# Optimization experiments

Hardware: AMD Instinct MI355X
Metric: run time of the kernel (lower is better)

Reference implementation:

```python
import jax, jax.numpy as jnp
import numpy as np

B, T, IN, H = 64, 512, 512, 512


def _lstm_scan(x_tbd, h0, c0, Wih, Whh, b):
    """Run an LSTMCell over time. x_tbd: [T,B,IN]. Returns hs [T,B,H], (h,c)."""
    def step(carry, x):
        h, c = carry
        g = x @ Wih.T + h @ Whh.T + b          # [B, 4H], gates in torch order i,f,g,o
        i, f, gg, o = jnp.split(g, 4, axis=-1)
        i = jax.nn.sigmoid(i)
        f = jax.nn.sigmoid(f)
        gg = jnp.tanh(gg)
        o = jax.nn.sigmoid(o)
        c = f * c + i * gg
        h = o * jnp.tanh(c)
        return (h, c), h
    (h, c), hs = jax.lax.scan(step, (h0, c0), x_tbd)
    return hs, h, c


def setup_inputs() -> dict:
    key = jax.random.key(0)
    ks = jax.random.split(key, 9)
    s = 1.0 / np.sqrt(H)
    inp = {
        "input": jax.random.normal(ks[0], (B, T, IN), dtype=jnp.float32),
        "enc_h": jax.random.normal(ks[1], (B, 2 * H), dtype=jnp.float32),
        "enc_c": jax.random.normal(ks[2], (B, 2 * H), dtype=jnp.float32),
        "Wih_f": jax.random.uniform(ks[3], (4 * H, IN), jnp.float32, -s, s),
        "Whh_f": jax.random.uniform(ks[4], (4 * H, H), jnp.float32, -s, s),
        "b_f": jax.random.uniform(ks[5], (4 * H,), jnp.float32, -s, s),
        "Wih_b": jax.random.uniform(ks[6], (4 * H, IN), jnp.float32, -s, s),
        "Whh_b": jax.random.uniform(ks[7], (4 * H, H), jnp.float32, -s, s),
        "b_b": jax.random.uniform(ks[8], (4 * H,), jnp.float32, -s, s),
    }
    return inp


def reference(input, enc_h, enc_c, Wih_f, Whh_f, b_f, Wih_b, Whh_b, b_b):
    # split encoder state into forward / backward halves (num_layers=1)
    h0_f, h0_b = enc_h[:, :H], enc_h[:, H:]
    c0_f, c0_b = enc_c[:, :H], enc_c[:, H:]

    x_f = jnp.swapaxes(input, 0, 1)                 # [T,B,IN]
    x_b = jnp.swapaxes(jnp.flip(input, axis=1), 0, 1)

    out_f, h_f, c_f = _lstm_scan(x_f, h0_f, c0_f, Wih_f, Whh_f, b_f)
    out_b, h_b, c_b = _lstm_scan(x_b, h0_b, c0_b, Wih_b, Whh_b, b_b)

    out_f = jnp.swapaxes(out_f, 0, 1)               # [B,T,H]
    out_b = jnp.flip(jnp.swapaxes(out_b, 0, 1), axis=1)
    out = jnp.concatenate([out_f, out_b], axis=2)   # [B,T,2H]

    h = jnp.concatenate([h_f, h_b], axis=1)         # [B,2H]
    c = jnp.concatenate([c_f, c_b], axis=1)
    return out, h, c
```

## Files before the change

### kernel.cpp

```cpp
#include <hip/hip_runtime.h>

typedef _Float16 h8 __attribute__((ext_vector_type(8)));
typedef _Float16 h4 __attribute__((ext_vector_type(4)));
typedef float    f4 __attribute__((ext_vector_type(4)));
typedef unsigned u4 __attribute__((ext_vector_type(4)));

#define NT     512
#define OUT0   33554432
#define SENT   0x7fc00000u

__device__ __forceinline__ float sigm(float x)  { return 1.0f / (1.0f + __expf(-x)); }
__device__ __forceinline__ float tanhf_(float x){ float e = __expf(2.0f * x); return 1.0f - 2.0f / (e + 1.0f); }


__global__ __launch_bounds__(256) void xconv_k(const float* __restrict__ x, _Float16* __restrict__ x16) {
    size_t i = ((size_t)blockIdx.x * 256 + threadIdx.x) * 4;
    f4 v = *(const f4*)(x + i);
    h4 o; o[0] = (_Float16)v[0]; o[1] = (_Float16)v[1]; o[2] = (_Float16)v[2]; o[3] = (_Float16)v[3];
    *(h4*)(x16 + i) = o;
}

__global__ __launch_bounds__(256) void wconv_k(const float* __restrict__ Wih_f, const float* __restrict__ Whh_f,
                                               const float* __restrict__ Wih_b, const float* __restrict__ Whh_b,
                                               _Float16* __restrict__ wcat) {
    size_t e = (size_t)blockIdx.x * 256 + threadIdx.x;
    int k4  = (int)(e & 255);
    int p   = (int)((e >> 8) & 2047);
    int dir = (int)(e >> 19);
    int gate = p & 3, j = p >> 2;
    int k = k4 * 4;
    const float* Wih = dir ? Wih_b : Wih_f;
    const float* Whh = dir ? Whh_b : Whh_f;
    f4 v;
    if (k < 512) v = *(const f4*)&Wih[((size_t)gate * 512 + j) * 512 + k];
    else         v = *(const f4*)&Whh[((size_t)gate * 512 + j) * 512 + (k - 512)];
    h4 o; o[0] = (_Float16)v[0]; o[1] = (_Float16)v[1]; o[2] = (_Float16)v[2]; o[3] = (_Float16)v[3];
    *(h4*)&wcat[(((size_t)dir * 2048) + p) * 1024 + k] = o;
}

__global__ __launch_bounds__(256) void inith_k(const float* __restrict__ enc_h, _Float16* __restrict__ h16) {
    int e = blockIdx.x * 256 + threadIdx.x;
    float v = enc_h[e];
    int b = e >> 10, q = e & 1023, dir = q >> 9, j = q & 511;
    h16[((size_t)(dir * 64 + b)) * 512 + j] = (_Float16)v;
}

__global__ __launch_bounds__(256) void fillnan_k(unsigned* __restrict__ o) {
    size_t i = ((size_t)blockIdx.x * 256 + threadIdx.x) * 4;
    u4 v; v[0] = SENT; v[1] = SENT; v[2] = SENT; v[3] = SENT;
    *(u4*)(o + i) = v;
}

__global__ __launch_bounds__(256, 1) void lstm_persist(
    const _Float16* __restrict__ x16, const _Float16* __restrict__ wcat,
    const float* __restrict__ b_f, const float* __restrict__ b_b,
    const float* __restrict__ enc_c,
    const _Float16* __restrict__ h16,
    float* __restrict__ out, float* __restrict__ hseg, float* __restrict__ cseg)
{
    const int bx  = blockIdx.x;
    const int dir = bx >> 7, mg = (bx >> 5) & 3, ng = bx & 31;
    const int b0 = mg * 16, p0 = ng * 64, j0 = ng * 16;
    const int tid = threadIdx.x, lane = tid & 63, kw = tid >> 6;
    const int l15 = lane & 15, koff = (lane >> 4) * 8;

    __shared__ float gbuf[2][4][16][68];

    f4 wx[4][4], wh[4][4];
    #pragma unroll
    for (int nt = 0; nt < 4; ++nt) {
        const _Float16* wrow = wcat + ((size_t)dir * 2048 + p0 + nt * 16 + l15) * 1024 + kw * 128 + koff;
        #pragma unroll
        for (int s = 0; s < 4; ++s) {
            wx[nt][s] = *(const f4*)(wrow + s * 32);
            wh[nt][s] = *(const f4*)(wrow + 512 + s * 32);
        }
    }
    #pragma unroll
    for (int nt = 0; nt < 4; ++nt)
        #pragma unroll
        for (int s = 0; s < 4; ++s) {
            asm volatile("" : "+v"(wx[nt][s]));
            asm volatile("" : "+v"(wh[nt][s]));
        }

    const int mb = tid >> 4, jj = tid & 15;
    const float* bias = dir ? b_b : b_f;
    const float bi = bias[0 * 512 + j0 + jj];
    const float bf = bias[1 * 512 + j0 + jj];
    const float bg = bias[2 * 512 + j0 + jj];
    const float bo = bias[3 * 512 + j0 + jj];
    float c = enc_c[(size_t)(b0 + mb) * 1024 + dir * 512 + j0 + jj];
    float hlast = 0.f;

    const _Float16* xbase = x16 + (size_t)(b0 + l15) * NT * 512 + kw * 128 + koff;

    f4 xf[4];
    {
        const _Float16* xp = xbase + (size_t)(dir ? (NT - 1) : 0) * 512;
        #pragma unroll
        for (int s = 0; s < 4; ++s) xf[s] = *(const f4*)(xp + s * 32);
    }

    for (int t = 0; t < NT; ++t) {
        const int tx = dir ? (NT - 1 - t) : t;

        f4 acc[4];
        #pragma unroll
        for (int nt = 0; nt < 4; ++nt) { acc[nt][0] = 0.f; acc[nt][1] = 0.f; acc[nt][2] = 0.f; acc[nt][3] = 0.f; }
        #pragma unroll
        for (int s = 0; s < 4; ++s) {
            h8 a = __builtin_bit_cast(h8, xf[s]);
            #pragma unroll
            for (int nt = 0; nt < 4; ++nt)
                acc[nt] = __builtin_amdgcn_mfma_f32_16x16x32_f16(a, __builtin_bit_cast(h8, wx[nt][s]), acc[nt], 0, 0, 0);
        }
        #pragma unroll
        for (int nt = 0; nt < 4; ++nt) asm volatile("" : "+v"(acc[nt]));

        h8 hfr[4];
        if (t == 0) {
            const _Float16* hp = h16 + (size_t)dir * 64 * 512 + (size_t)(b0 + l15) * 512 + kw * 128 + koff;
            #pragma unroll
            for (int s = 0; s < 4; ++s) hfr[s] = *(const h8*)(hp + s * 32);
        } else {
            const int txp = dir ? (NT - t) : (t - 1);
            const unsigned* hp32 = (const unsigned*)(out
                + ((size_t)(b0 + l15) * NT + txp) * 1024 + (size_t)dir * 512 + kw * 128 + koff);
            u4 q0, q1, q2, q3, q4, q5, q6, q7;
            int ok;
            do {
                asm volatile(
                    "global_load_dwordx4 %0, %8, off sc0 sc1\n\t"
                    "global_load_dwordx4 %1, %8, off offset:16 sc0 sc1\n\t"
                    "global_load_dwordx4 %2, %8, off offset:128 sc0 sc1\n\t"
                    "global_load_dwordx4 %3, %8, off offset:144 sc0 sc1\n\t"
                    "global_load_dwordx4 %4, %8, off offset:256 sc0 sc1\n\t"
                    "global_load_dwordx4 %5, %8, off offset:272 sc0 sc1\n\t"
                    "global_load_dwordx4 %6, %8, off offset:384 sc0 sc1\n\t"
                    "global_load_dwordx4 %7, %8, off offset:400 sc0 sc1\n\t"
                    "s_waitcnt vmcnt(0)"
                    : "=&v"(q0), "=&v"(q1), "=&v"(q2), "=&v"(q3),
                      "=&v"(q4), "=&v"(q5), "=&v"(q6), "=&v"(q7)
                    : "v"(hp32) : "memory");
                ok = (q0[0] != SENT) & (q0[1] != SENT) & (q0[2] != SENT) & (q0[3] != SENT)
                   & (q1[0] != SENT) & (q1[1] != SENT) & (q1[2] != SENT) & (q1[3] != SENT)
                   & (q2[0] != SENT) & (q2[1] != SENT) & (q2[2] != SENT) & (q2[3] != SENT)
                   & (q3[0] != SENT) & (q3[1] != SENT) & (q3[2] != SENT) & (q3[3] != SENT)
                   & (q4[0] != SENT) & (q4[1] != SENT) & (q4[2] != SENT) & (q4[3] != SENT)
                   & (q5[0] != SENT) & (q5[1] != SENT) & (q5[2] != SENT) & (q5[3] != SENT)
                   & (q6[0] != SENT) & (q6[1] != SENT) & (q6[2] != SENT) & (q6[3] != SENT)
                   & (q7[0] != SENT) & (q7[1] != SENT) & (q7[2] != SENT) & (q7[3] != SENT);
            } while (!__all(ok));
            f4 v0 = __builtin_bit_cast(f4, q0), v1 = __builtin_bit_cast(f4, q1);
            f4 v2 = __builtin_bit_cast(f4, q2), v3 = __builtin_bit_cast(f4, q3);
            f4 v4 = __builtin_bit_cast(f4, q4), v5 = __builtin_bit_cast(f4, q5);
            f4 v6 = __builtin_bit_cast(f4, q6), v7 = __builtin_bit_cast(f4, q7);
            #pragma unroll
            for (int e = 0; e < 4; ++e) {
                hfr[0][e] = (_Float16)v0[e]; hfr[0][4 + e] = (_Float16)v1[e];
                hfr[1][e] = (_Float16)v2[e]; hfr[1][4 + e] = (_Float16)v3[e];
                hfr[2][e] = (_Float16)v4[e]; hfr[2][4 + e] = (_Float16)v5[e];
                hfr[3][e] = (_Float16)v6[e]; hfr[3][4 + e] = (_Float16)v7[e];
            }
        }

        #pragma unroll
        for (int s = 0; s < 4; ++s)
            #pragma unroll
            for (int nt = 0; nt < 4; ++nt)
                acc[nt] = __builtin_amdgcn_mfma_f32_16x16x32_f16(hfr[s], __builtin_bit_cast(h8, wh[nt][s]), acc[nt], 0, 0, 0);

        if (t + 1 < NT) {
            const _Float16* xp = xbase + (size_t)(dir ? (NT - 2 - t) : (t + 1)) * 512;
            #pragma unroll
            for (int s = 0; s < 4; ++s) xf[s] = *(const f4*)(xp + s * 32);
        }

        float (*gb)[16][68] = gbuf[t & 1];
        #pragma unroll
        for (int nt = 0; nt < 4; ++nt)
            #pragma unroll
            for (int r = 0; r < 4; ++r)
                gb[kw][(lane >> 4) * 4 + r][nt * 16 + l15] = acc[nt][r];
        __syncthreads();

        float gi = bi, gf = bf, gg = bg, go = bo;
        #pragma unroll
        for (int w = 0; w < 4; ++w) {
            gi += gb[w][mb][jj * 4 + 0];
            gf += gb[w][mb][jj * 4 + 1];
            gg += gb[w][mb][jj * 4 + 2];
            go += gb[w][mb][jj * 4 + 3];
        }
        float i_ = sigm(gi), f_ = sigm(gf), o_ = sigm(go), g_ = tanhf_(gg);
        c = f_ * c + i_ * g_;
        float h = o_ * tanhf_(c);
        hlast = h;

        {
            float* od = out + ((size_t)(b0 + mb) * NT + tx) * 1024 + (size_t)(dir * 512 + j0 + jj);
            asm volatile("global_store_dword %0, %1, off sc0 sc1" :: "v"(od), "v"(h) : "memory");
        }
    }

    asm volatile("s_waitcnt vmcnt(0)" ::: "memory");

    hseg[(size_t)(b0 + mb) * 1024 + dir * 512 + j0 + jj] = hlast;
    cseg[(size_t)(b0 + mb) * 1024 + dir * 512 + j0 + jj] = c;
}


extern "C" void kernel_launch(void* const* d_in, const int* in_sizes, int n_in,
                              void* d_out, int out_size, void* d_ws, size_t ws_size,
                              hipStream_t stream) {
    const float* xin   = (const float*)d_in[0];
    const float* enc_h = (const float*)d_in[1];
    const float* enc_c = (const float*)d_in[2];
    const float* Wih_f = (const float*)d_in[3];
    const float* Whh_f = (const float*)d_in[4];
    const float* b_f   = (const float*)d_in[5];
    const float* Wih_b = (const float*)d_in[6];
    const float* Whh_b = (const float*)d_in[7];
    const float* b_b   = (const float*)d_in[8];

    float* out  = (float*)d_out;
    float* hseg = out + OUT0;
    float* cseg = hseg + 65536;

    const size_t X16_BYTES  = (size_t)64 * 512 * 512 * 2;
    const size_t WCAT_BYTES = (size_t)2 * 2048 * 1024 * 2;

    _Float16* x16  = (_Float16*)d_ws;
    _Float16* wcat = (_Float16*)((char*)d_ws + X16_BYTES);
    _Float16* h16  = (_Float16*)((char*)d_ws + X16_BYTES + WCAT_BYTES);

    xconv_k<<<dim3(16384), dim3(256), 0, stream>>>(xin, x16);
    wconv_k<<<dim3(4096), dim3(256), 0, stream>>>(Wih_f, Whh_f, Wih_b, Whh_b, wcat);
    inith_k<<<dim3(256), dim3(256), 0, stream>>>(enc_h, h16);
    fillnan_k<<<dim3(32768), dim3(256), 0, stream>>>((unsigned*)out);
    lstm_persist<<<dim3(256), dim3(256), 0, stream>>>(x16, wcat, b_f, b_b, enc_c,
                                                      h16, out, hseg, cseg);
}
```

Before: 1.783 ms.

## Replace NaN-sentinel output polling with tagged fp16 double-buffered h ring

Cross-block hidden-state exchange now goes through a small double-buffered ring in workspace, where each word packs an fp16 h with a step tag. Consumers issue the poll loads early and overlap them with the x-projection MFMAs. This removes the full-output NaN fill kernel and polling on the large strided output tensor. The output is written with plain stores, and the block-to-work mapping is interleaved so different directions and batch groups spread across the device. The cost is an extra store per step and more careful memory ordering.

```diff
diff --git a/kernel.cpp b/kernel.cpp
--- a/kernel.cpp
+++ b/kernel.cpp
@@ -7,7 +7,6 @@
 
 #define NT     512
 #define OUT0   33554432
-#define SENT   0x7fc00000u
 
 __device__ __forceinline__ float sigm(float x)  { return 1.0f / (1.0f + __expf(-x)); }
 __device__ __forceinline__ float tanhf_(float x){ float e = __expf(2.0f * x); return 1.0f - 2.0f / (e + 1.0f); }
@@ -38,28 +37,25 @@
     *(h4*)&wcat[(((size_t)dir * 2048) + p) * 1024 + k] = o;
 }
 
-__global__ __launch_bounds__(256) void inith_k(const float* __restrict__ enc_h, _Float16* __restrict__ h16) {
+__global__ __launch_bounds__(256) void initring_k(const float* __restrict__ enc_h, unsigned* __restrict__ rb) {
     int e = blockIdx.x * 256 + threadIdx.x;
     float v = enc_h[e];
     int b = e >> 10, q = e & 1023, dir = q >> 9, j = q & 511;
-    h16[((size_t)(dir * 64 + b)) * 512 + j] = (_Float16)v;
-}
-
-__global__ __launch_bounds__(256) void fillnan_k(unsigned* __restrict__ o) {
-    size_t i = ((size_t)blockIdx.x * 256 + threadIdx.x) * 4;
-    u4 v; v[0] = SENT; v[1] = SENT; v[2] = SENT; v[3] = SENT;
-    *(u4*)(o + i) = v;
+    unsigned short hb = __builtin_bit_cast(unsigned short, (_Float16)v);
+    size_t idx = ((size_t)dir * 64 + b) * 512 + j;
+    rb[idx]         = (unsigned)hb;
+    rb[idx + 65536] = 0xFFFF0000u;
 }
 
 __global__ __launch_bounds__(256, 1) void lstm_persist(
     const _Float16* __restrict__ x16, const _Float16* __restrict__ wcat,
     const float* __restrict__ b_f, const float* __restrict__ b_b,
-    const float* __restrict__ enc_c,
-    const _Float16* __restrict__ h16,
+    const float* __restrict__ enc_c, unsigned* __restrict__ rb,
     float* __restrict__ out, float* __restrict__ hseg, float* __restrict__ cseg)
 {
     const int bx  = blockIdx.x;
-    const int dir = bx >> 7, mg = (bx >> 5) & 3, ng = bx & 31;
+    const int grp = bx & 7;
+    const int dir = grp >> 2, mg = grp & 3, ng = bx >> 3;
     const int b0 = mg * 16, p0 = ng * 64, j0 = ng * 16;
     const int tid = threadIdx.x, lane = tid & 63, kw = tid >> 6;
     const int l15 = lane & 15, koff = (lane >> 4) * 8;
@@ -102,8 +98,26 @@
         for (int s = 0; s < 4; ++s) xf[s] = *(const f4*)(xp + s * 32);
     }
 
+    const unsigned* pbase = rb + (size_t)dir * 32768 + (size_t)(b0 + l15) * 512 + kw * 128 + koff;
+    unsigned* sbase = rb + (size_t)dir * 32768 + (size_t)(b0 + mb) * 512 + (j0 + jj);
+
     for (int t = 0; t < NT; ++t) {
         const int tx = dir ? (NT - 1 - t) : t;
+        const unsigned* pp = pbase + (size_t)(t & 1) * 65536;
+
+        u4 q0, q1, q2, q3, q4, q5, q6, q7;
+        asm volatile(
+            "global_load_dwordx4 %0, %8, off sc0 sc1\n\t"
+            "global_load_dwordx4 %1, %8, off offset:16 sc0 sc1\n\t"
+            "global_load_dwordx4 %2, %8, off offset:128 sc0 sc1\n\t"
+            "global_load_dwordx4 %3, %8, off offset:144 sc0 sc1\n\t"
+            "global_load_dwordx4 %4, %8, off offset:256 sc0 sc1\n\t"
+            "global_load_dwordx4 %5, %8, off offset:272 sc0 sc1\n\t"
+            "global_load_dwordx4 %6, %8, off offset:384 sc0 sc1\n\t"
+            "global_load_dwordx4 %7, %8, off offset:400 sc0 sc1"
+            : "=&v"(q0), "=&v"(q1), "=&v"(q2), "=&v"(q3),
+              "=&v"(q4), "=&v"(q5), "=&v"(q6), "=&v"(q7)
+            : "v"(pp) : "memory");
 
         f4 acc[4];
         #pragma unroll
@@ -117,52 +131,57 @@
         }
         #pragma unroll
         for (int nt = 0; nt < 4; ++nt) asm volatile("" : "+v"(acc[nt]));
+        __builtin_amdgcn_sched_barrier(0);
+
+        const unsigned tagx = (unsigned)t << 16;
+        for (;;) {
+            asm volatile("s_waitcnt vmcnt(0)" ::: "memory");
+            __builtin_amdgcn_sched_barrier(0);
+            int ok = ((q0[0]^tagx)<0x10000u) & ((q0[1]^tagx)<0x10000u) & ((q0[2]^tagx)<0x10000u) & ((q0[3]^tagx)<0x10000u)
+                   & ((q1[0]^tagx)<0x10000u) & ((q1[1]^tagx)<0x10000u) & ((q1[2]^tagx)<0x10000u) & ((q1[3]^tagx)<0x10000u)
+                   & ((q2[0]^tagx)<0x10000u) & ((q2[1]^tagx)<0x10000u) & ((q2[2]^tagx)<0x10000u) & ((q2[3]^tagx)<0x10000u)
+                   & ((q3[0]^tagx)<0x10000u) & ((q3[1]^tagx)<0x10000u) & ((q3[2]^tagx)<0x10000u) & ((q3[3]^tagx)<0x10000u)
+                   & ((q4[0]^tagx)<0x10000u) & ((q4[1]^tagx)<0x10000u) & ((q4[2]^tagx)<0x10000u) & ((q4[3]^tagx)<0x10000u)
+                   & ((q5[0]^tagx)<0x10000u) & ((q5[1]^tagx)<0x10000u) & ((q5[2]^tagx)<0x10000u) & ((q5[3]^tagx)<0x10000u)
+                   & ((q6[0]^tagx)<0x10000u) & ((q6[1]^tagx)<0x10000u) & ((q6[2]^tagx)<0x10000u) & ((q6[3]^tagx)<0x10000u)
+                   & ((q7[0]^tagx)<0x10000u) & ((q7[1]^tagx)<0x10000u) & ((q7[2]^tagx)<0x10000u) & ((q7[3]^tagx)<0x10000u);
+            if (__all(ok)) break;
+            asm volatile(
+                "global_load_dwordx4 %0, %8, off sc0 sc1\n\t"
+                "global_load_dwordx4 %1, %8, off offset:16 sc0 sc1\n\t"
+                "global_load_dwordx4 %2, %8, off offset:128 sc0 sc1\n\t"
+                "global_load_dwordx4 %3, %8, off offset:144 sc0 sc1\n\t"
+                "global_load_dwordx4 %4, %8, off offset:256 sc0 sc1\n\t"
+                "global_load_dwordx4 %5, %8, off offset:272 sc0 sc1\n\t"
+                "global_load_dwordx4 %6, %8, off offset:384 sc0 sc1\n\t"
+                "global_load_dwordx4 %7, %8, off offset:400 sc0 sc1\n\t"
+                "s_waitcnt vmcnt(0)"
+                : "=&v"(q0), "=&v"(q1), "=&v"(q2), "=&v"(q3),
+                  "=&v"(q4), "=&v"(q5), "=&v"(q6), "=&v"(q7)
+                : "v"(pp) : "memory");
+        }
+
+        if (t + 1 < NT) {
+            const _Float16* xp = xbase + (size_t)(dir ? (NT - 2 - t) : (t + 1)) * 512;
+            #pragma unroll
+            for (int s = 0; s < 4; ++s) xf[s] = *(const f4*)(xp + s * 32);
+        }
 
         h8 hfr[4];
-        if (t == 0) {
-            const _Float16* hp = h16 + (size_t)dir * 64 * 512 + (size_t)(b0 + l15) * 512 + kw * 128 + koff;
-            #pragma unroll
-            for (int s = 0; s < 4; ++s) hfr[s] = *(const h8*)(hp + s * 32);
-        } else {
-            const int txp = dir ? (NT - t) : (t - 1);
-            const unsigned* hp32 = (const unsigned*)(out
-                + ((size_t)(b0 + l15) * NT + txp) * 1024 + (size_t)dir * 512 + kw * 128 + koff);
-            u4 q0, q1, q2, q3, q4, q5, q6, q7;
-            int ok;
-            do {
-                asm volatile(
-                    "global_load_dwordx4 %0, %8, off sc0 sc1\n\t"
-                    "global_load_dwordx4 %1, %8, off offset:16 sc0 sc1\n\t"
-                    "global_load_dwordx4 %2, %8, off offset:128 sc0 sc1\n\t"
-                    "global_load_dwordx4 %3, %8, off offset:144 sc0 sc1\n\t"
-                    "global_load_dwordx4 %4, %8, off offset:256 sc0 sc1\n\t"
-                    "global_load_dwordx4 %5, %8, off offset:272 sc0 sc1\n\t"
-                    "global_load_dwordx4 %6, %8, off offset:384 sc0 sc1\n\t"
-                    "global_load_dwordx4 %7, %8, off offset:400 sc0 sc1\n\t"
-                    "s_waitcnt vmcnt(0)"
-                    : "=&v"(q0), "=&v"(q1), "=&v"(q2), "=&v"(q3),
-                      "=&v"(q4), "=&v"(q5), "=&v"(q6), "=&v"(q7)
-                    : "v"(hp32) : "memory");
-                ok = (q0[0] != SENT) & (q0[1] != SENT) & (q0[2] != SENT) & (q0[3] != SENT)
-                   & (q1[0] != SENT) & (q1[1] != SENT) & (q1[2] != SENT) & (q1[3] != SENT)
-                   & (q2[0] != SENT) & (q2[1] != SENT) & (q2[2] != SENT) & (q2[3] != SENT)
-                   & (q3[0] != SENT) & (q3[1] != SENT) & (q3[2] != SENT) & (q3[3] != SENT)
-                   & (q4[0] != SENT) & (q4[1] != SENT) & (q4[2] != SENT) & (q4[3] != SENT)
-                   & (q5[0] != SENT) & (q5[1] != SENT) & (q5[2] != SENT) & (q5[3] != SENT)
-                   & (q6[0] != SENT) & (q6[1] != SENT) & (q6[2] != SENT) & (q6[3] != SENT)
-                   & (q7[0] != SENT) & (q7[1] != SENT) & (q7[2] != SENT) & (q7[3] != SENT);
-            } while (!__all(ok));
-            f4 v0 = __builtin_bit_cast(f4, q0), v1 = __builtin_bit_cast(f4, q1);
-            f4 v2 = __builtin_bit_cast(f4, q2), v3 = __builtin_bit_cast(f4, q3);
-            f4 v4 = __builtin_bit_cast(f4, q4), v5 = __builtin_bit_cast(f4, q5);
-            f4 v6 = __builtin_bit_cast(f4, q6), v7 = __builtin_bit_cast(f4, q7);
-            #pragma unroll
-            for (int e = 0; e < 4; ++e) {
-                hfr[0][e] = (_Float16)v0[e]; hfr[0][4 + e] = (_Float16)v1[e];
-                hfr[1][e] = (_Float16)v2[e]; hfr[1][4 + e] = (_Float16)v3[e];
-                hfr[2][e] = (_Float16)v4[e]; hfr[2][4 + e] = (_Float16)v5[e];
-                hfr[3][e] = (_Float16)v6[e]; hfr[3][4 + e] = (_Float16)v7[e];
-            }
+        {
+            u4 w;
+            w[0] = (q0[0]&0xffffu)|(q0[1]<<16); w[1] = (q0[2]&0xffffu)|(q0[3]<<16);
+            w[2] = (q1[0]&0xffffu)|(q1[1]<<16); w[3] = (q1[2]&0xffffu)|(q1[3]<<16);
+            hfr[0] = __builtin_bit_cast(h8, w);
+            w[0] = (q2[0]&0xffffu)|(q2[1]<<16); w[1] = (q2[2]&0xffffu)|(q2[3]<<16);
+            w[2] = (q3[0]&0xffffu)|(q3[1]<<16); w[3] = (q3[2]&0xffffu)|(q3[3]<<16);
+            hfr[1] = __builtin_bit_cast(h8, w);
+            w[0] = (q4[0]&0xffffu)|(q4[1]<<16); w[1] = (q4[2]&0xffffu)|(q4[3]<<16);
+            w[2] = (q5[0]&0xffffu)|(q5[1]<<16); w[3] = (q5[2]&0xffffu)|(q5[3]<<16);
+            hfr[2] = __builtin_bit_cast(h8, w);
+            w[0] = (q6[0]&0xffffu)|(q6[1]<<16); w[1] = (q6[2]&0xffffu)|(q6[3]<<16);
+            w[2] = (q7[0]&0xffffu)|(q7[1]<<16); w[3] = (q7[2]&0xffffu)|(q7[3]<<16);
+            hfr[3] = __builtin_bit_cast(h8, w);
         }
 
         #pragma unroll
@@ -170,12 +189,6 @@
             #pragma unroll
             for (int nt = 0; nt < 4; ++nt)
                 acc[nt] = __builtin_amdgcn_mfma_f32_16x16x32_f16(hfr[s], __builtin_bit_cast(h8, wh[nt][s]), acc[nt], 0, 0, 0);
-
-        if (t + 1 < NT) {
-            const _Float16* xp = xbase + (size_t)(dir ? (NT - 2 - t) : (t + 1)) * 512;
-            #pragma unroll
-            for (int s = 0; s < 4; ++s) xf[s] = *(const f4*)(xp + s * 32);
-        }
 
         float (*gb)[16][68] = gbuf[t & 1];
         #pragma unroll
@@ -199,9 +212,12 @@
         hlast = h;
 
         {
-            float* od = out + ((size_t)(b0 + mb) * NT + tx) * 1024 + (size_t)(dir * 512 + j0 + jj);
-            asm volatile("global_store_dword %0, %1, off sc0 sc1" :: "v"(od), "v"(h) : "memory");
-        }
+            unsigned short hb = __builtin_bit_cast(unsigned short, (_Float16)h);
+            unsigned uv = ((unsigned)(t + 1) << 16) | (unsigned)hb;
+            unsigned* rd = sbase + (size_t)((t + 1) & 1) * 65536;
+            asm volatile("global_store_dword %0, %1, off sc0 sc1" :: "v"(rd), "v"(uv) : "memory");
+        }
+        out[((size_t)(b0 + mb) * NT + tx) * 1024 + (size_t)(dir * 512 + j0 + jj)] = h;
     }
 
     asm volatile("s_waitcnt vmcnt(0)" ::: "memory");
@@ -233,12 +249,11 @@
 
     _Float16* x16  = (_Float16*)d_ws;
     _Float16* wcat = (_Float16*)((char*)d_ws + X16_BYTES);
-    _Float16* h16  = (_Float16*)((char*)d_ws + X16_BYTES + WCAT_BYTES);
+    unsigned* rb   = (unsigned*)((char*)d_ws + X16_BYTES + WCAT_BYTES);
 
     xconv_k<<<dim3(16384), dim3(256), 0, stream>>>(xin, x16);
     wconv_k<<<dim3(4096), dim3(256), 0, stream>>>(Wih_f, Whh_f, Wih_b, Whh_b, wcat);
-    inith_k<<<dim3(256), dim3(256), 0, stream>>>(enc_h, h16);
-    fillnan_k<<<dim3(32768), dim3(256), 0, stream>>>((unsigned*)out);
+    initring_k<<<dim3(256), dim3(256), 0, stream>>>(enc_h, rb);
     lstm_persist<<<dim3(256), dim3(256), 0, stream>>>(x16, wcat, b_f, b_b, enc_c,
-                                                      h16, out, hseg, cseg);
-}
+                                                      rb, out, hseg, cseg);
+}
```

Result: slower. 2.027 ms (+13.7%).

## Interleave two batch groups per block to overlap polling latency with compute

Applied to the files above, without the earlier changes.

Each persistent block now handles two 16-row batch groups, A and B, in alternation, so the grid shrinks from 256 to 128 blocks. While one group computes its recurrent MFMAs and gate math, the poll load for the other group's previous hidden state is already issued, which hides the cross-block global-memory round trip. The cost is twice the serial per-step work per block and half the CUs in use, in exchange for overlapping synchronisation latency. The LDS barrier is replaced with an explicit lgkmcnt wait plus s_barrier.

```diff
diff --git a/kernel.cpp b/kernel.cpp
--- a/kernel.cpp
+++ b/kernel.cpp
@@ -51,6 +51,53 @@
     *(u4*)(o + i) = v;
 }
 
+#define ISSUE_POLL(pp)                                                  \
+    asm volatile(                                                       \
+        "global_load_dwordx4 %0, %8, off sc0 sc1\n\t"                   \
+        "global_load_dwordx4 %1, %8, off offset:16 sc0 sc1\n\t"         \
+        "global_load_dwordx4 %2, %8, off offset:128 sc0 sc1\n\t"        \
+        "global_load_dwordx4 %3, %8, off offset:144 sc0 sc1\n\t"        \
+        "global_load_dwordx4 %4, %8, off offset:256 sc0 sc1\n\t"        \
+        "global_load_dwordx4 %5, %8, off offset:272 sc0 sc1\n\t"        \
+        "global_load_dwordx4 %6, %8, off offset:384 sc0 sc1\n\t"        \
+        "global_load_dwordx4 %7, %8, off offset:400 sc0 sc1"            \
+        : "=&v"(q0), "=&v"(q1), "=&v"(q2), "=&v"(q3),                   \
+          "=&v"(q4), "=&v"(q5), "=&v"(q6), "=&v"(q7)                    \
+        : "v"(pp) : "memory")
+
+#define POLL_SPIN(pp)                                                            \
+    for (;;) {                                                                   \
+        asm volatile("s_waitcnt vmcnt(0)" ::: "memory");                         \
+        __builtin_amdgcn_sched_barrier(0);                         \
+        int ok = (q0[0]!=SENT)&(q0[1]!=SENT)&(q0[2]!=SENT)&(q0[3]!=SENT)         \
+               & (q1[0]!=SENT)&(q1[1]!=SENT)&(q1[2]!=SENT)&(q1[3]!=SENT)         \
+               & (q2[0]!=SENT)&(q2[1]!=SENT)&(q2[2]!=SENT)&(q2[3]!=SENT)         \
+               & (q3[0]!=SENT)&(q3[1]!=SENT)&(q3[2]!=SENT)&(q3[3]!=SENT)         \
+               & (q4[0]!=SENT)&(q4[1]!=SENT)&(q4[2]!=SENT)&(q4[3]!=SENT)         \
+               & (q5[0]!=SENT)&(q5[1]!=SENT)&(q5[2]!=SENT)&(q5[3]!=SENT)         \
+               & (q6[0]!=SENT)&(q6[1]!=SENT)&(q6[2]!=SENT)&(q6[3]!=SENT)         \
+               & (q7[0]!=SENT)&(q7[1]!=SENT)&(q7[2]!=SENT)&(q7[3]!=SENT);        \
+        if (__all(ok)) break;                                                    \
+        ISSUE_POLL(pp);                                                          \
+    }
+
+#define PACK_HFR(hfr)                                                            \
+    {                                                                            \
+        f4 v0 = __builtin_bit_cast(f4, q0), v1 = __builtin_bit_cast(f4, q1);     \
+        f4 v2 = __builtin_bit_cast(f4, q2), v3 = __builtin_bit_cast(f4, q3);     \
+        f4 v4 = __builtin_bit_cast(f4, q4), v5 = __builtin_bit_cast(f4, q5);     \
+        f4 v6 = __builtin_bit_cast(f4, q6), v7 = __builtin_bit_cast(f4, q7);     \
+        _Pragma("unroll")                                                        \
+        for (int e = 0; e < 4; ++e) {                                            \
+            hfr[0][e] = (_Float16)v0[e]; hfr[0][4 + e] = (_Float16)v1[e];        \
+            hfr[1][e] = (_Float16)v2[e]; hfr[1][4 + e] = (_Float16)v3[e];        \
+            hfr[2][e] = (_Float16)v4[e]; hfr[2][4 + e] = (_Float16)v5[e];        \
+            hfr[3][e] = (_Float16)v6[e]; hfr[3][4 + e] = (_Float16)v7[e];        \
+        }                                                                        \
+    }
+
+#define BARRIER_LDS() asm volatile("s_waitcnt lgkmcnt(0)\n\ts_barrier" ::: "memory")
+
 __global__ __launch_bounds__(256, 1) void lstm_persist(
     const _Float16* __restrict__ x16, const _Float16* __restrict__ wcat,
     const float* __restrict__ b_f, const float* __restrict__ b_b,
@@ -59,8 +106,9 @@
     float* __restrict__ out, float* __restrict__ hseg, float* __restrict__ cseg)
 {
     const int bx  = blockIdx.x;
-    const int dir = bx >> 7, mg = (bx >> 5) & 3, ng = bx & 31;
-    const int b0 = mg * 16, p0 = ng * 64, j0 = ng * 16;
+    const int dir = bx >> 6, pr = (bx >> 5) & 1, ng = bx & 31;
+    const int b0A = pr * 32, b0B = pr * 32 + 16;
+    const int p0 = ng * 64, j0 = ng * 16;
     const int tid = threadIdx.x, lane = tid & 63, kw = tid >> 6;
     const int l15 = lane & 15, koff = (lane >> 4) * 8;
 
@@ -90,124 +138,167 @@
     const float bf = bias[1 * 512 + j0 + jj];
     const float bg = bias[2 * 512 + j0 + jj];
     const float bo = bias[3 * 512 + j0 + jj];
-    float c = enc_c[(size_t)(b0 + mb) * 1024 + dir * 512 + j0 + jj];
-    float hlast = 0.f;
-
-    const _Float16* xbase = x16 + (size_t)(b0 + l15) * NT * 512 + kw * 128 + koff;
-
-    f4 xf[4];
+    float cA = enc_c[(size_t)(b0A + mb) * 1024 + dir * 512 + j0 + jj];
+    float cB = enc_c[(size_t)(b0B + mb) * 1024 + dir * 512 + j0 + jj];
+    float hlastA = 0.f, hlastB = 0.f;
+
+    const _Float16* xbaseA = x16 + (size_t)(b0A + l15) * NT * 512 + kw * 128 + koff;
+    const _Float16* xbaseB = x16 + (size_t)(b0B + l15) * NT * 512 + kw * 128 + koff;
+
+    f4 xfA[4], xfB[4];
     {
-        const _Float16* xp = xbase + (size_t)(dir ? (NT - 1) : 0) * 512;
-        #pragma unroll
-        for (int s = 0; s < 4; ++s) xf[s] = *(const f4*)(xp + s * 32);
-    }
+        const size_t t0 = (size_t)(dir ? (NT - 1) : 0) * 512;
+        #pragma unroll
+        for (int s = 0; s < 4; ++s) { xfA[s] = *(const f4*)(xbaseA + t0 + s * 32); xfB[s] = *(const f4*)(xbaseB + t0 + s * 32); }
+    }
+
+    const float* pA = out + (size_t)(b0A + l15) * NT * 1024 + dir * 512 + kw * 128 + koff;
+    const float* pB = out + (size_t)(b0B + l15) * NT * 1024 + dir * 512 + kw * 128 + koff;
+    float* oA = out + (size_t)(b0A + mb) * NT * 1024 + dir * 512 + j0 + jj;
+    float* oB = out + (size_t)(b0B + mb) * NT * 1024 + dir * 512 + j0 + jj;
+
+    u4 q0, q1, q2, q3, q4, q5, q6, q7;
 
     for (int t = 0; t < NT; ++t) {
-        const int tx = dir ? (NT - 1 - t) : t;
+        const int tx  = dir ? (NT - 1 - t) : t;
+        const int txp = dir ? (NT - t)     : t - 1;
 
         f4 acc[4];
         #pragma unroll
         for (int nt = 0; nt < 4; ++nt) { acc[nt][0] = 0.f; acc[nt][1] = 0.f; acc[nt][2] = 0.f; acc[nt][3] = 0.f; }
         #pragma unroll
         for (int s = 0; s < 4; ++s) {
-            h8 a = __builtin_bit_cast(h8, xf[s]);
+            h8 a = __builtin_bit_cast(h8, xfA[s]);
             #pragma unroll
             for (int nt = 0; nt < 4; ++nt)
                 acc[nt] = __builtin_amdgcn_mfma_f32_16x16x32_f16(a, __builtin_bit_cast(h8, wx[nt][s]), acc[nt], 0, 0, 0);
         }
         #pragma unroll
         for (int nt = 0; nt < 4; ++nt) asm volatile("" : "+v"(acc[nt]));
-
-        h8 hfr[4];
+        __builtin_amdgcn_sched_barrier(0);
+
+        h8 hfrA[4];
         if (t == 0) {
-            const _Float16* hp = h16 + (size_t)dir * 64 * 512 + (size_t)(b0 + l15) * 512 + kw * 128 + koff;
-            #pragma unroll
-            for (int s = 0; s < 4; ++s) hfr[s] = *(const h8*)(hp + s * 32);
+            const _Float16* hp = h16 + (size_t)dir * 64 * 512 + (size_t)(b0A + l15) * 512 + kw * 128 + koff;
+            #pragma unroll
+            for (int s = 0; s < 4; ++s) hfrA[s] = *(const h8*)(hp + s * 32);
         } else {
-            const int txp = dir ? (NT - t) : (t - 1);
-            const unsigned* hp32 = (const unsigned*)(out
-                + ((size_t)(b0 + l15) * NT + txp) * 1024 + (size_t)dir * 512 + kw * 128 + koff);
-            u4 q0, q1, q2, q3, q4, q5, q6, q7;
-            int ok;
-            do {
-                asm volatile(
-                    "global_load_dwordx4 %0, %8, off sc0 sc1\n\t"
-                    "global_load_dwordx4 %1, %8, off offset:16 sc0 sc1\n\t"
-                    "global_load_dwordx4 %2, %8, off offset:128 sc0 sc1\n\t"
-                    "global_load_dwordx4 %3, %8, off offset:144 sc0 sc1\n\t"
-                    "global_load_dwordx4 %4, %8, off offset:256 sc0 sc1\n\t"
-                    "global_load_dwordx4 %5, %8, off offset:272 sc0 sc1\n\t"
-                    "global_load_dwordx4 %6, %8, off offset:384 sc0 sc1\n\t"
-                    "global_load_dwordx4 %7, %8, off offset:400 sc0 sc1\n\t"
-                    "s_waitcnt vmcnt(0)"
-                    : "=&v"(q0), "=&v"(q1), "=&v"(q2), "=&v"(q3),
-                      "=&v"(q4), "=&v"(q5), "=&v"(q6), "=&v"(q7)
-                    : "v"(hp32) : "memory");
-                ok = (q0[0] != SENT) & (q0[1] != SENT) & (q0[2] != SENT) & (q0[3] != SENT)
-                   & (q1[0] != SENT) & (q1[1] != SENT) & (q1[2] != SENT) & (q1[3] != SENT)
-                   & (q2[0] != SENT) & (q2[1] != SENT) & (q2[2] != SENT) & (q2[3] != SENT)
-                   & (q3[0] != SENT) & (q3[1] != SENT) & (q3[2] != SENT) & (q3[3] != SENT)
-                   & (q4[0] != SENT) & (q4[1] != SENT) & (q4[2] != SENT) & (q4[3] != SENT)
-                   & (q5[0] != SENT) & (q5[1] != SENT) & (q5[2] != SENT) & (q5[3] != SENT)
-                   & (q6[0] != SENT) & (q6[1] != SENT) & (q6[2] != SENT) & (q6[3] != SENT)
-                   & (q7[0] != SENT) & (q7[1] != SENT) & (q7[2] != SENT) & (q7[3] != SENT);
-            } while (!__all(ok));
-            f4 v0 = __builtin_bit_cast(f4, q0), v1 = __builtin_bit_cast(f4, q1);
-            f4 v2 = __builtin_bit_cast(f4, q2), v3 = __builtin_bit_cast(f4, q3);
-            f4 v4 = __builtin_bit_cast(f4, q4), v5 = __builtin_bit_cast(f4, q5);
-            f4 v6 = __builtin_bit_cast(f4, q6), v7 = __builtin_bit_cast(f4, q7);
-            #pragma unroll
-            for (int e = 0; e < 4; ++e) {
-                hfr[0][e] = (_Float16)v0[e]; hfr[0][4 + e] = (_Float16)v1[e];
-                hfr[1][e] = (_Float16)v2[e]; hfr[1][4 + e] = (_Float16)v3[e];
-                hfr[2][e] = (_Float16)v4[e]; hfr[2][4 + e] = (_Float16)v5[e];
-                hfr[3][e] = (_Float16)v6[e]; hfr[3][4 + e] = (_Float16)v7[e];
+            const unsigned* pp = (const unsigned*)(pA + (size_t)txp * 1024);
+            POLL_SPIN(pp);
+            PACK_HFR(hfrA);
+            const unsigned* ppB = (const unsigned*)(pB + (size_t)txp * 1024);
+            ISSUE_POLL(ppB);
+            __builtin_amdgcn_sched_barrier(0);
+        }
+
+        #pragma unroll
+        for (int s = 0; s < 4; ++s)
+            #pragma unroll
+            for (int nt = 0; nt < 4; ++nt)
+                acc[nt] = __builtin_amdgcn_mfma_f32_16x16x32_f16(hfrA[s], __builtin_bit_cast(h8, wh[nt][s]), acc[nt], 0, 0, 0);
+
+        if (t + 1 < NT) {
+            const _Float16* xp = xbaseA + (size_t)(dir ? (NT - 2 - t) : (t + 1)) * 512;
+            #pragma unroll
+            for (int s = 0; s < 4; ++s) xfA[s] = *(const f4*)(xp + s * 32);
+        }
+
+        #pragma unroll
+        for (int nt = 0; nt < 4; ++nt)
+            #pragma unroll
+            for (int r = 0; r < 4; ++r)
+                gbuf[0][kw][(lane >> 4) * 4 + r][nt * 16 + l15] = acc[nt][r];
+        BARRIER_LDS();
+
+        {
+            float gi = bi, gf = bf, gg = bg, go = bo;
+            #pragma unroll
+            for (int w = 0; w < 4; ++w) {
+                gi += gbuf[0][w][mb][jj * 4 + 0];
+                gf += gbuf[0][w][mb][jj * 4 + 1];
+                gg += gbuf[0][w][mb][jj * 4 + 2];
+                go += gbuf[0][w][mb][jj * 4 + 3];
             }
+            float i_ = sigm(gi), f_ = sigm(gf), o_ = sigm(go), g_ = tanhf_(gg);
+            cA = f_ * cA + i_ * g_;
+            float h = o_ * tanhf_(cA);
+            hlastA = h;
+            float* od = oA + (size_t)tx * 1024;
+            asm volatile("global_store_dword %0, %1, off sc0 sc1" :: "v"(od), "v"(h) : "memory");
+        }
+
+        #pragma unroll
+        for (int nt = 0; nt < 4; ++nt) { acc[nt][0] = 0.f; acc[nt][1] = 0.f; acc[nt][2] = 0.f; acc[nt][3] = 0.f; }
+        #pragma unroll
+        for (int s = 0; s < 4; ++s) {
+            h8 a = __builtin_bit_cast(h8, xfB[s]);
+            #pragma unroll
+            for (int nt = 0; nt < 4; ++nt)
+                acc[nt] = __builtin_amdgcn_mfma_f32_16x16x32_f16(a, __builtin_bit_cast(h8, wx[nt][s]), acc[nt], 0, 0, 0);
+        }
+        #pragma unroll
+        for (int nt = 0; nt < 4; ++nt) asm volatile("" : "+v"(acc[nt]));
+        __builtin_amdgcn_sched_barrier(0);
+
+        h8 hfrB[4];
+        if (t == 0) {
+            const _Float16* hp = h16 + (size_t)dir * 64 * 512 + (size_t)(b0B + l15) * 512 + kw * 128 + koff;
+            #pragma unroll
+            for (int s = 0; s < 4; ++s) hfrB[s] = *(const h8*)(hp + s * 32);
+        } else {
+            const unsigned* pp = (const unsigned*)(pB + (size_t)txp * 1024);
+            POLL_SPIN(pp);
+            PACK_HFR(hfrB);
+        }
+        if (t + 1 < NT) {
+            const unsigned* ppA = (const unsigned*)(pA + (size_t)tx * 1024);
+            ISSUE_POLL(ppA);
+            __builtin_amdgcn_sched_barrier(0);
         }
 
         #pragma unroll
         for (int s = 0; s < 4; ++s)
             #pragma unroll
             for (int nt = 0; nt < 4; ++nt)
-                acc[nt] = __builtin_amdgcn_mfma_f32_16x16x32_f16(hfr[s], __builtin_bit_cast(h8, wh[nt][s]), acc[nt], 0, 0, 0);
+                acc[nt] = __builtin_amdgcn_mfma_f32_16x16x32_f16(hfrB[s], __builtin_bit_cast(h8, wh[nt][s]), acc[nt], 0, 0, 0);
 
         if (t + 1 < NT) {
-            const _Float16* xp = xbase + (size_t)(dir ? (NT - 2 - t) : (t + 1)) * 512;
-            #pragma unroll
-            for (int s = 0; s < 4; ++s) xf[s] = *(const f4*)(xp + s * 32);
-        }
-
-        float (*gb)[16][68] = gbuf[t & 1];
+            const _Float16* xp = xbaseB + (size_t)(dir ? (NT - 2 - t) : (t + 1)) * 512;
+            #pragma unroll
+            for (int s = 0; s < 4; ++s) xfB[s] = *(const f4*)(xp + s * 32);
+        }
+
         #pragma unroll
         for (int nt = 0; nt < 4; ++nt)
             #pragma unroll
             for (int r = 0; r < 4; ++r)
-                gb[kw][(lane >> 4) * 4 + r][nt * 16 + l15] = acc[nt][r];
-        __syncthreads();
-
-        float gi = bi, gf = bf, gg = bg, go = bo;
-        #pragma unroll
-        for (int w = 0; w < 4; ++w) {
-            gi += gb[w][mb][jj * 4 + 0];
-            gf += gb[w][mb][jj * 4 + 1];
-            gg += gb[w][mb][jj * 4 + 2];
-            go += gb[w][mb][jj * 4 + 3];
-        }
-        float i_ = sigm(gi), f_ = sigm(gf), o_ = sigm(go), g_ = tanhf_(gg);
-        c = f_ * c + i_ * g_;
-        float h = o_ * tanhf_(c);
-        hlast = h;
+                gbuf[1][kw][(lane >> 4) * 4 + r][nt * 16 + l15] = acc[nt][r];
+        BARRIER_LDS();
 
         {
-            float* od = out + ((size_t)(b0 + mb) * NT + tx) * 1024 + (size_t)(dir * 512 + j0 + jj);
+            float gi = bi, gf = bf, gg = bg, go = bo;
+            #pragma unroll
+            for (int w = 0; w < 4; ++w) {
+                gi += gbuf[1][w][mb][jj * 4 + 0];
+                gf += gbuf[1][w][mb][jj * 4 + 1];
+                gg += gbuf[1][w][mb][jj * 4 + 2];
+                go += gbuf[1][w][mb][jj * 4 + 3];
+            }
+            float i_ = sigm(gi), f_ = sigm(gf), o_ = sigm(go), g_ = tanhf_(gg);
+            cB = f_ * cB + i_ * g_;
+            float h = o_ * tanhf_(cB);
+            hlastB = h;
+            float* od = oB + (size_t)tx * 1024;
             asm volatile("global_store_dword %0, %1, off sc0 sc1" :: "v"(od), "v"(h) : "memory");
         }
     }
 
     asm volatile("s_waitcnt vmcnt(0)" ::: "memory");
 
-    hseg[(size_t)(b0 + mb) * 1024 + dir * 512 + j0 + jj] = hlast;
-    cseg[(size_t)(b0 + mb) * 1024 + dir * 512 + j0 + jj] = c;
+    hseg[(size_t)(b0A + mb) * 1024 + dir * 512 + j0 + jj] = hlastA;
+    cseg[(size_t)(b0A + mb) * 1024 + dir * 512 + j0 + jj] = cA;
+    hseg[(size_t)(b0B + mb) * 1024 + dir * 512 + j0 + jj] = hlastB;
+    cseg[(size_t)(b0B + mb) * 1024 + dir * 512 + j0 + jj] = cB;
 }
 
 
@@ -239,6 +330,6 @@
     wconv_k<<<dim3(4096), dim3(256), 0, stream>>>(Wih_f, Whh_f, Wih_b, Whh_b, wcat);
     inith_k<<<dim3(256), dim3(256), 0, stream>>>(enc_h, h16);
     fillnan_k<<<dim3(32768), dim3(256), 0, stream>>>((unsigned*)out);
-    lstm_persist<<<dim3(256), dim3(256), 0, stream>>>(x16, wcat, b_f, b_b, enc_c,
+    lstm_persist<<<dim3(128), dim3(256), 0, stream>>>(x16, wcat, b_f, b_b, enc_c,
                                                       h16, out, hseg, cseg);
 }
```

Result: slower. 2.673 ms (+49.9%).
